# Kernel optimization log

Measured on AMD Instinct MI355X. Metric: run time of the kernel, lower is better.

The kernel has to match this reference:

```python
import jax, jax.numpy as jnp
import numpy as np

N_NODES = 100000
N_EDGES = 1600000
F_IN, HIDDEN, N_CLASS = 64, 48, 40


def setup_inputs() -> dict:
    key = jax.random.key(0)
    ks = jax.random.split(key, 9)
    def glorot(k, fi, fo):
        s = (6.0 / (fi + fo)) ** 0.5
        return jax.random.uniform(k, (fi, fo), jnp.float32, -s, s)
    return {
        "x": jax.random.normal(ks[0], (N_NODES, F_IN), jnp.float32),
        "edge_index": jax.random.randint(ks[1], (2, N_EDGES), 0, N_NODES, jnp.int64),
        "edge_weight": jax.random.uniform(ks[2], (N_EDGES,), jnp.float32),
        "W1": glorot(ks[3], F_IN, HIDDEN),   # ARMAConv init_weight (K=1)
        "V1": glorot(ks[4], F_IN, HIDDEN),   # ARMAConv root_weight
        "b1": jnp.zeros((HIDDEN,), jnp.float32),
        "W2": glorot(ks[5], HIDDEN, N_CLASS),
        "V2": glorot(ks[6], HIDDEN, N_CLASS),
        "b2": jnp.zeros((N_CLASS,), jnp.float32),
    }


def _arma_conv(x, W, V, b, src, dst, norm, num_nodes):
    # out = ReLU( A_norm @ (x @ W) + x @ V + b )   (num_stacks=1, num_layers=1)
    h = x @ W                                   # [N, F_out]
    msg = h[src] * norm[:, None]                # gather + scale  [E, F_out]
    agg = jax.ops.segment_sum(msg, dst, num_segments=num_nodes)  # scatter-add
    return jax.nn.relu(agg + x @ V + b)


def reference(x, edge_index, edge_weight, W1, V1, b1, W2, V2, b2):
    num_nodes = x.shape[0]
    src, dst = edge_index[0], edge_index[1]
    # gcn_norm, add_self_loops=False: D^{-1/2} A D^{-1/2}
    deg = jax.ops.segment_sum(edge_weight, dst, num_segments=num_nodes)
    dinv = jnp.where(deg > 0, jax.lax.rsqrt(jnp.where(deg > 0, deg, 1.0)), 0.0)
    norm = dinv[src] * edge_weight * dinv[dst]
    # eval mode: input dropout is identity
    h = _arma_conv(x, W1, V1, b1, src, dst, norm, num_nodes)
    h = _arma_conv(h, W2, V2, b2, src, dst, norm, num_nodes)
    return jax.nn.log_softmax(h, axis=-1)
```

## Files before the change

### kernel.cpp

```cpp
#include <hip/hip_runtime.h>
#include <math.h>


constexpr int F_IN = 64;
constexpr int HIDDEN = 48;
constexpr int N_CLASS = 40;
constexpr int CHUNK = 8192;
constexpr int BIN_SHIFT = 9;
constexpr int BIN_CAP = 9216;
constexpr int CSR_CAP = 12288;

typedef __attribute__((ext_vector_type(8))) short bf16x8;
typedef __attribute__((ext_vector_type(4))) float f32x4;

__device__ __forceinline__ short bfr(float f) {
    unsigned u = __float_as_uint(f);
    return (short)((u + 0x7fffu + ((u >> 16) & 1u)) >> 16);
}
__device__ __forceinline__ unsigned pack_bf2(float a, float b) {
    unsigned ua = __float_as_uint(a), ub = __float_as_uint(b);
    ua = (ua + 0x7fffu + ((ua >> 16) & 1u)) >> 16;
    ub = (ub + 0x7fffu + ((ub >> 16) & 1u)) >> 16;
    return ua | (ub << 16);
}
__device__ __forceinline__ float2 unpack_bf2(unsigned u) {
    return make_float2(__uint_as_float(u << 16), __uint_as_float(u & 0xffff0000u));
}
__device__ __forceinline__ bf16x8 cvt8(float4 f0, float4 f1) {
    bf16x8 r;
    r[0] = bfr(f0.x); r[1] = bfr(f0.y); r[2] = bfr(f0.z); r[3] = bfr(f0.w);
    r[4] = bfr(f1.x); r[5] = bfr(f1.y); r[6] = bfr(f1.z); r[7] = bfr(f1.w);
    return r;
}

__global__ void init_cursor(int* __restrict__ binCursor) {
    binCursor[threadIdx.x] = (int)threadIdx.x * BIN_CAP;
}

__global__ __launch_bounds__(256) void gemm1_kernel(
    const float* __restrict__ X, const float* __restrict__ W,
    const float* __restrict__ V, const float* __restrict__ b,
    unsigned* __restrict__ XWp, unsigned* __restrict__ AGGp, int N) {
    __shared__ char smem[36864];
    short* sWT = (short*)smem;
    float* ep = (float*)(smem + 12288);
    int tid = threadIdx.x;
    for (int i = tid; i < 96 * 64; i += 256) {
        int c = i >> 6, k = i & 63;
        float v = (c < 48) ? W[k * 48 + c] : V[k * 48 + (c - 48)];
        sWT[i] = bfr(v);
    }
    __syncthreads();

    int lane = tid & 63, wv = tid >> 6;
    int m = lane & 15, quad = lane >> 4;
    int nb0 = (int)blockIdx.x * 64;
    int n = nb0 + wv * 16 + m;

    bf16x8 a0, a1;
    if (n < N) {
        const float4* xr = (const float4*)(X + (size_t)n * 64 + quad * 8);
        a0 = cvt8(xr[0], xr[1]);
        const float4* xr2 = (const float4*)(X + (size_t)n * 64 + 32 + quad * 8);
        a1 = cvt8(xr2[0], xr2[1]);
    } else {
        for (int j = 0; j < 8; ++j) { a0[j] = 0; a1[j] = 0; }
    }

    f32x4 acc[6];
#pragma unroll
    for (int ct = 0; ct < 6; ++ct) acc[ct] = (f32x4){0.f, 0.f, 0.f, 0.f};
#pragma unroll
    for (int ct = 0; ct < 6; ++ct) {
        bf16x8 b0 = *(const bf16x8*)(sWT + (ct * 16 + m) * 64 + quad * 8);
        bf16x8 b1 = *(const bf16x8*)(sWT + (ct * 16 + m) * 64 + 32 + quad * 8);
        acc[ct] = __builtin_amdgcn_mfma_f32_16x16x32_bf16(a0, b0, acc[ct], 0, 0, 0);
        acc[ct] = __builtin_amdgcn_mfma_f32_16x16x32_bf16(a1, b1, acc[ct], 0, 0, 0);
    }
#pragma unroll
    for (int ct = 0; ct < 6; ++ct)
#pragma unroll
        for (int r = 0; r < 4; ++r)
            ep[(wv * 16 + quad * 4 + r) * 96 + ct * 16 + m] = acc[ct][r];
    __syncthreads();
    for (int i = tid; i < 64 * 24; i += 256) {
        int r = i / 24, c2 = i - r * 24;
        int node = nb0 + r;
        if (node >= N) continue;
        float w0 = ep[r * 96 + 2 * c2], w1 = ep[r * 96 + 2 * c2 + 1];
        XWp[node * 24 + c2] = pack_bf2(w0, w1);
        float v0 = ep[r * 96 + 48 + 2 * c2], v1 = ep[r * 96 + 48 + 2 * c2 + 1];
        float2 bb = ((const float2*)b)[c2];
        AGGp[node * 24 + c2] = pack_bf2(v0 + bb.x, v1 + bb.y);
    }
}

__global__ __launch_bounds__(256) void binscatter(
    const int* __restrict__ src, const int* __restrict__ dst,
    const float* __restrict__ w, int* __restrict__ binCursor,
    int2* __restrict__ binned, int E) {
    __shared__ int sx[CHUNK];
    __shared__ int sw[CHUNK];
    __shared__ unsigned char sbin[CHUNK];
    __shared__ int hist[256];
    int tid = threadIdx.x;
    hist[tid] = 0;
    __syncthreads();
    long long e0 = (long long)blockIdx.x * CHUNK;
    int M = (int)min((long long)CHUNK, (long long)E - e0);
    for (int i = tid; i < M; i += 256) {
        int d = dst[e0 + i];
        int bn = d >> BIN_SHIFT;
        sx[i] = ((d & 511) << 17) | src[e0 + i];
        sw[i] = __float_as_int(w[e0 + i]);
        sbin[i] = (unsigned char)bn;
        atomicAdd(&hist[bn], 1);
    }
    __syncthreads();
    int base = atomicAdd(&binCursor[tid], hist[tid]);
    __syncthreads();
    hist[tid] = base;
    __syncthreads();
    for (int i = tid; i < M; i += 256) {
        int p = atomicAdd(&hist[sbin[i]], 1);
        binned[p] = make_int2(sx[i], sw[i]);
    }
}

__global__ __launch_bounds__(512) void build_csr(const int2* __restrict__ binned,
                                                 const int* __restrict__ binCursor,
                                                 int* __restrict__ rowBeg,
                                                 int* __restrict__ rowEnd,
                                                 float* __restrict__ dinv,
                                                 unsigned* __restrict__ csr,
                                                 unsigned* __restrict__ XW1p, int N) {
    __shared__ int sx[CSR_CAP];
    __shared__ int sw[CSR_CAP];
    __shared__ int cntL[512];
    __shared__ float degL[512];
    __shared__ int scanL[512];
    int b = blockIdx.x, tid = threadIdx.x;
    int e0 = b * BIN_CAP;
    int M = min(binCursor[b] - e0, BIN_CAP);
    cntL[tid] = 0;
    degL[tid] = 0.f;
    __syncthreads();
    for (int i = tid; i < M; i += 512) {
        int2 p = binned[e0 + i];
        sx[i] = p.x;
        sw[i] = p.y;
        int dl = ((unsigned)p.x) >> 17;
        atomicAdd(&cntL[dl], 1);
        atomicAdd(&degL[dl], __int_as_float(p.y));
    }
    __syncthreads();
    int v = cntL[tid];
    scanL[tid] = v;
    __syncthreads();
#pragma unroll
    for (int o = 1; o < 512; o <<= 1) {
        int u = (tid >= o) ? scanL[tid - o] : 0;
        __syncthreads();
        scanL[tid] += u;
        __syncthreads();
    }
    int excl = scanL[tid] - v;
    int node = (b << BIN_SHIFT) + tid;
    float dg = degL[tid];
    float dv = dg > 0.f ? rsqrtf(dg) : 0.f;
    if (node < N) {
        rowBeg[node] = e0 + excl;
        rowEnd[node] = e0 + excl + v;
        dinv[node] = dv;
    }
    cntL[tid] = e0 + excl;
    degL[tid] = dv;
    __syncthreads();
    for (int i = tid; i < M; i += 512) {
        int px = sx[i], pw = sw[i];
        int dl = ((unsigned)px) >> 17;
        int pos = atomicAdd(&cntL[dl], 1);
        float wn = __int_as_float(pw) * degL[dl];
        unsigned uw = __float_as_uint(wn);
        uw = (uw + 0x7fffu + ((uw >> 16) & 1u)) >> 16;
        csr[pos] = ((unsigned)(px & 0x1FFFF) << 15) | uw;
    }
    int nb0 = b << BIN_SHIFT;
    for (int i = tid; i < 512 * 24; i += 512) {
        int nl = i / 24, c = i - nl * 24;
        int nn = nb0 + nl;
        if (nn >= N) break;
        float dvn = degL[nl];
        float2 u = unpack_bf2(XW1p[nn * 24 + c]);
        XW1p[nn * 24 + c] = pack_bf2(u.x * dvn, u.y * dvn);
    }
}

template <int W>
__device__ __forceinline__ float4 row_accum2(const unsigned* __restrict__ XWp,
                                             const unsigned* __restrict__ csr,
                                             int j, int end, int c, float4 s) {
    while (j < end && (j & 3)) {
        unsigned p = csr[j++];
        uint2 u = *(const uint2*)(XWp + (p >> 15) * W + c);
        float nr = __uint_as_float((p & 0x7FFFu) << 16);
        float2 x0 = unpack_bf2(u.x), x1 = unpack_bf2(u.y);
        s.x = fmaf(x0.x, nr, s.x); s.y = fmaf(x0.y, nr, s.y);
        s.z = fmaf(x1.x, nr, s.z); s.w = fmaf(x1.y, nr, s.w);
    }
    for (; j + 4 <= end; j += 4) {
        uint4 p4 = *(const uint4*)(csr + j);
        uint2 u0 = *(const uint2*)(XWp + (p4.x >> 15) * W + c);
        uint2 u1 = *(const uint2*)(XWp + (p4.y >> 15) * W + c);
        uint2 u2 = *(const uint2*)(XWp + (p4.z >> 15) * W + c);
        uint2 u3 = *(const uint2*)(XWp + (p4.w >> 15) * W + c);
        float n0 = __uint_as_float((p4.x & 0x7FFFu) << 16);
        float n1 = __uint_as_float((p4.y & 0x7FFFu) << 16);
        float n2 = __uint_as_float((p4.z & 0x7FFFu) << 16);
        float n3 = __uint_as_float((p4.w & 0x7FFFu) << 16);
        float2 a0 = unpack_bf2(u0.x), b0 = unpack_bf2(u0.y);
        float2 a1 = unpack_bf2(u1.x), b1 = unpack_bf2(u1.y);
        float2 a2 = unpack_bf2(u2.x), b2 = unpack_bf2(u2.y);
        float2 a3 = unpack_bf2(u3.x), b3 = unpack_bf2(u3.y);
        s.x = fmaf(a0.x, n0, s.x); s.y = fmaf(a0.y, n0, s.y);
        s.z = fmaf(b0.x, n0, s.z); s.w = fmaf(b0.y, n0, s.w);
        s.x = fmaf(a1.x, n1, s.x); s.y = fmaf(a1.y, n1, s.y);
        s.z = fmaf(b1.x, n1, s.z); s.w = fmaf(b1.y, n1, s.w);
        s.x = fmaf(a2.x, n2, s.x); s.y = fmaf(a2.y, n2, s.y);
        s.z = fmaf(b2.x, n2, s.z); s.w = fmaf(b2.y, n2, s.w);
        s.x = fmaf(a3.x, n3, s.x); s.y = fmaf(a3.y, n3, s.y);
        s.z = fmaf(b3.x, n3, s.z); s.w = fmaf(b3.y, n3, s.w);
    }
    for (; j < end; ++j) {
        unsigned p = csr[j];
        uint2 u = *(const uint2*)(XWp + (p >> 15) * W + c);
        float nr = __uint_as_float((p & 0x7FFFu) << 16);
        float2 x0 = unpack_bf2(u.x), x1 = unpack_bf2(u.y);
        s.x = fmaf(x0.x, nr, s.x); s.y = fmaf(x0.y, nr, s.y);
        s.z = fmaf(x1.x, nr, s.z); s.w = fmaf(x1.y, nr, s.w);
    }
    return s;
}

__global__ __launch_bounds__(384) void pull_agg(const unsigned* __restrict__ XWp,
                                                const unsigned* __restrict__ csr,
                                                const int* __restrict__ rowBeg,
                                                const int* __restrict__ rowEnd,
                                                const unsigned* __restrict__ AGG1p,
                                                unsigned* __restrict__ H1p, int N) {
    int t = blockIdx.x * blockDim.x + threadIdx.x;
    int n = t / 12, c1 = t - n * 12;
    if (n >= N) return;
    int c = 2 * c1;
    uint2 a = *(const uint2*)(AGG1p + n * 24 + c);
    float2 f0 = unpack_bf2(a.x), f1 = unpack_bf2(a.y);
    float4 s = make_float4(f0.x, f0.y, f1.x, f1.y);
    s = row_accum2<24>(XWp, csr, rowBeg[n], rowEnd[n], c, s);
    uint2 o;
    o.x = pack_bf2(fmaxf(s.x, 0.f), fmaxf(s.y, 0.f));
    o.y = pack_bf2(fmaxf(s.z, 0.f), fmaxf(s.w, 0.f));
    *(uint2*)(H1p + n * 24 + c) = o;
}

__global__ __launch_bounds__(256) void gemm2_kernel(
    const short* __restrict__ H1, const float* __restrict__ W,
    const float* __restrict__ V, const float* __restrict__ b,
    const float* __restrict__ dinv, unsigned* __restrict__ XWp,
    unsigned* __restrict__ AGGp, int N) {
    __shared__ char smem[30720];
    short* sWT = (short*)smem;
    float* ep = (float*)(smem + 10240);
    int tid = threadIdx.x;
    for (int i = tid; i < 80 * 64; i += 256) {
        int c = i >> 6, k = i & 63;
        float v = 0.f;
        if (k < 48) v = (c < 40) ? W[k * 40 + c] : V[k * 40 + (c - 40)];
        sWT[i] = bfr(v);
    }
    __syncthreads();

    int lane = tid & 63, wv = tid >> 6;
    int m = lane & 15, quad = lane >> 4;
    int nb0 = (int)blockIdx.x * 64;
    int n = nb0 + wv * 16 + m;

    bf16x8 a0, a1;
    if (n < N) {
        a0 = *(const bf16x8*)(H1 + (size_t)n * 48 + quad * 8);
        if (quad < 2) {
            a1 = *(const bf16x8*)(H1 + (size_t)n * 48 + 32 + quad * 8);
        } else {
            for (int j = 0; j < 8; ++j) a1[j] = 0;
        }
    } else {
        for (int j = 0; j < 8; ++j) { a0[j] = 0; a1[j] = 0; }
    }

    f32x4 acc[5];
#pragma unroll
    for (int ct = 0; ct < 5; ++ct) acc[ct] = (f32x4){0.f, 0.f, 0.f, 0.f};
#pragma unroll
    for (int ct = 0; ct < 5; ++ct) {
        bf16x8 b0 = *(const bf16x8*)(sWT + (ct * 16 + m) * 64 + quad * 8);
        bf16x8 b1 = *(const bf16x8*)(sWT + (ct * 16 + m) * 64 + 32 + quad * 8);
        acc[ct] = __builtin_amdgcn_mfma_f32_16x16x32_bf16(a0, b0, acc[ct], 0, 0, 0);
        acc[ct] = __builtin_amdgcn_mfma_f32_16x16x32_bf16(a1, b1, acc[ct], 0, 0, 0);
    }
#pragma unroll
    for (int ct = 0; ct < 5; ++ct)
#pragma unroll
        for (int r = 0; r < 4; ++r)
            ep[(wv * 16 + quad * 4 + r) * 80 + ct * 16 + m] = acc[ct][r];
    __syncthreads();
    for (int i = tid; i < 64 * 20; i += 256) {
        int r = i / 20, c2 = i - r * 20;
        int node = nb0 + r;
        if (node >= N) continue;
        float dv = dinv[node];
        float w0 = ep[r * 80 + 2 * c2], w1 = ep[r * 80 + 2 * c2 + 1];
        XWp[node * 20 + c2] = pack_bf2(w0 * dv, w1 * dv);
        float v0 = ep[r * 80 + 40 + 2 * c2], v1 = ep[r * 80 + 40 + 2 * c2 + 1];
        float2 bb = ((const float2*)b)[c2];
        AGGp[node * 20 + c2] = pack_bf2(v0 + bb.x, v1 + bb.y);
    }
}

__global__ __launch_bounds__(320) void pull_ls(const unsigned* __restrict__ XWp,
                                               const unsigned* __restrict__ csr,
                                               const int* __restrict__ rowBeg,
                                               const int* __restrict__ rowEnd,
                                               const unsigned* __restrict__ AGG2p,
                                               float* __restrict__ out, int N) {
    __shared__ float4 sbuf[32 * 10];
    __shared__ float sl[32];
    int tid = threadIdx.x;
    int nl = tid / 10, c1 = tid - nl * 10;
    int n = blockIdx.x * 32 + nl;
    int c = 2 * c1;
    float4 s = make_float4(0.f, 0.f, 0.f, 0.f);
    if (n < N) {
        uint2 a = *(const uint2*)(AGG2p + n * 20 + c);
        float2 f0 = unpack_bf2(a.x), f1 = unpack_bf2(a.y);
        s = make_float4(f0.x, f0.y, f1.x, f1.y);
        s = row_accum2<20>(XWp, csr, rowBeg[n], rowEnd[n], c, s);
    }
    sbuf[nl * 10 + c1] = s;
    __syncthreads();
    if (tid < 32) {
        float m = 0.f;
        for (int k = 0; k < 10; ++k) {
            float4 v = sbuf[tid * 10 + k];
            m = fmaxf(m, fmaxf(fmaxf(v.x, v.y), fmaxf(v.z, v.w)));
        }
        float sum = 0.f;
        for (int k = 0; k < 10; ++k) {
            float4 v = sbuf[tid * 10 + k];
            sum += expf(fmaxf(v.x, 0.f) - m) + expf(fmaxf(v.y, 0.f) - m) +
                   expf(fmaxf(v.z, 0.f) - m) + expf(fmaxf(v.w, 0.f) - m);
        }
        sl[tid] = m + logf(sum);
    }
    __syncthreads();
    if (n < N) {
        float l = sl[nl];
        ((float4*)out)[n * 10 + c1] =
            make_float4(fmaxf(s.x, 0.f) - l, fmaxf(s.y, 0.f) - l,
                        fmaxf(s.z, 0.f) - l, fmaxf(s.w, 0.f) - l);
    }
}

extern "C" void kernel_launch(void* const* d_in, const int* in_sizes, int n_in,
                              void* d_out, int out_size, void* d_ws, size_t ws_size,
                              hipStream_t stream) {
    const float* x  = (const float*)d_in[0];
    const int*   ei = (const int*)d_in[1];
    const float* ew = (const float*)d_in[2];
    const float* W1 = (const float*)d_in[3];
    const float* V1 = (const float*)d_in[4];
    const float* b1 = (const float*)d_in[5];
    const float* W2 = (const float*)d_in[6];
    const float* V2 = (const float*)d_in[7];
    const float* b2 = (const float*)d_in[8];
    float* out = (float*)d_out;

    const int N = in_sizes[0] / F_IN;
    const int E = in_sizes[2];
    const int* src = ei;
    const int* dst = ei + E;

    char* ws = (char*)d_ws;
    size_t off = 0;
    auto carve = [&](size_t bytes) {
        void* p = ws + off;
        off = (off + bytes + 255) & ~size_t(255);
        return p;
    };
    int*      binCursor = (int*)carve(256 * 4);
    int*      rowBeg    = (int*)carve((size_t)N * 4);
    int*      rowEnd    = (int*)carve((size_t)N * 4);
    float*    dinv      = (float*)carve((size_t)N * 4);
    int2*     binned    = (int2*)carve((size_t)256 * BIN_CAP * 8);
    unsigned* csr       = (unsigned*)carve((size_t)256 * BIN_CAP * 4);
    unsigned* xW1p      = (unsigned*)carve((size_t)N * 24 * 4);
    unsigned* agg1p     = (unsigned*)carve((size_t)N * 24 * 4);
    unsigned* h1p       = (unsigned*)carve((size_t)N * 24 * 4);
    unsigned* xW2p      = (unsigned*)carve((size_t)N * 20 * 4);
    unsigned* agg2p     = (unsigned*)carve((size_t)N * 20 * 4);

    const int B = 256;
    auto cdiv = [](long long a, long long b) { return (int)((a + b - 1) / b); };
    const int nSc = cdiv(E, CHUNK);
    const int nBins = (N + (1 << BIN_SHIFT) - 1) >> BIN_SHIFT;
    const int nGemmBlocks = cdiv(N, 64);

    init_cursor<<<1, 256, 0, stream>>>(binCursor);
    binscatter<<<nSc, B, 0, stream>>>(src, dst, ew, binCursor, binned, E);
    gemm1_kernel<<<nGemmBlocks, B, 0, stream>>>(x, W1, V1, b1, xW1p, agg1p, N);
    build_csr<<<nBins, 512, 0, stream>>>(binned, binCursor, rowBeg, rowEnd,
                                         dinv, csr, xW1p, N);

    pull_agg<<<cdiv((long long)N * 12, 384), 384, 0, stream>>>(xW1p, csr, rowBeg,
                                                               rowEnd, agg1p, h1p, N);

    gemm2_kernel<<<nGemmBlocks, B, 0, stream>>>((const short*)h1p, W2, V2, b2,
                                                dinv, xW2p, agg2p, N);

    pull_ls<<<cdiv(N, 32), 320, 0, stream>>>(xW2p, csr, rowBeg, rowEnd,
                                             agg2p, out, N);
}
```

Baseline: 275.2 us.

## Split each node's edge list across two lanes in pull aggregation kernels

Both pull kernels (layer 1 aggregation and layer 2 with log-softmax) now assign two threads per feature-pair slice of a node. The two threads interleave 4-edge chunks of the CSR row and combine their partial sums with a lane shuffle. This doubles the thread count and the number of independent gather streams, aiming to hide gather latency on rows of about 16 edges. In exchange it adds shuffle and branching work, duplicate CSR index loads per lane pair, and narrower per-thread writes.

New measurement: 293.4 us. +6.6%, slower.

```diff
diff --git a/kernel.cpp b/kernel.cpp
--- a/kernel.cpp
+++ b/kernel.cpp
@@ -197,18 +197,24 @@
 }
 
 template <int W>
-__device__ __forceinline__ float4 row_accum2(const unsigned* __restrict__ XWp,
-                                             const unsigned* __restrict__ csr,
-                                             int j, int end, int c, float4 s) {
-    while (j < end && (j & 3)) {
-        unsigned p = csr[j++];
-        uint2 u = *(const uint2*)(XWp + (p >> 15) * W + c);
-        float nr = __uint_as_float((p & 0x7FFFu) << 16);
-        float2 x0 = unpack_bf2(u.x), x1 = unpack_bf2(u.y);
-        s.x = fmaf(x0.x, nr, s.x); s.y = fmaf(x0.y, nr, s.y);
-        s.z = fmaf(x1.x, nr, s.z); s.w = fmaf(x1.y, nr, s.w);
-    }
-    for (; j + 4 <= end; j += 4) {
+__device__ __forceinline__ float4 row_accum_split(const unsigned* __restrict__ XWp,
+                                                  const unsigned* __restrict__ csr,
+                                                  int beg, int end, int s, int c,
+                                                  float4 acc) {
+    int ja = min((beg + 3) & ~3, end);
+    if (s == 0) {
+        for (int j = beg; j < ja; ++j) {
+            unsigned p = csr[j];
+            uint2 u = *(const uint2*)(XWp + (p >> 15) * W + c);
+            float nr = __uint_as_float((p & 0x7FFFu) << 16);
+            float2 x0 = unpack_bf2(u.x), x1 = unpack_bf2(u.y);
+            acc.x = fmaf(x0.x, nr, acc.x); acc.y = fmaf(x0.y, nr, acc.y);
+            acc.z = fmaf(x1.x, nr, acc.z); acc.w = fmaf(x1.y, nr, acc.w);
+        }
+    }
+    int nch = (end - ja) >> 2;
+    for (int ck = s; ck < nch; ck += 2) {
+        int j = ja + 4 * ck;
         uint4 p4 = *(const uint4*)(csr + j);
         uint2 u0 = *(const uint2*)(XWp + (p4.x >> 15) * W + c);
         uint2 u1 = *(const uint2*)(XWp + (p4.y >> 15) * W + c);
@@ -222,24 +228,27 @@
         float2 a1 = unpack_bf2(u1.x), b1 = unpack_bf2(u1.y);
         float2 a2 = unpack_bf2(u2.x), b2 = unpack_bf2(u2.y);
         float2 a3 = unpack_bf2(u3.x), b3 = unpack_bf2(u3.y);
-        s.x = fmaf(a0.x, n0, s.x); s.y = fmaf(a0.y, n0, s.y);
-        s.z = fmaf(b0.x, n0, s.z); s.w = fmaf(b0.y, n0, s.w);
-        s.x = fmaf(a1.x, n1, s.x); s.y = fmaf(a1.y, n1, s.y);
-        s.z = fmaf(b1.x, n1, s.z); s.w = fmaf(b1.y, n1, s.w);
-        s.x = fmaf(a2.x, n2, s.x); s.y = fmaf(a2.y, n2, s.y);
-        s.z = fmaf(b2.x, n2, s.z); s.w = fmaf(b2.y, n2, s.w);
-        s.x = fmaf(a3.x, n3, s.x); s.y = fmaf(a3.y, n3, s.y);
-        s.z = fmaf(b3.x, n3, s.z); s.w = fmaf(b3.y, n3, s.w);
-    }
-    for (; j < end; ++j) {
-        unsigned p = csr[j];
-        uint2 u = *(const uint2*)(XWp + (p >> 15) * W + c);
-        float nr = __uint_as_float((p & 0x7FFFu) << 16);
-        float2 x0 = unpack_bf2(u.x), x1 = unpack_bf2(u.y);
-        s.x = fmaf(x0.x, nr, s.x); s.y = fmaf(x0.y, nr, s.y);
-        s.z = fmaf(x1.x, nr, s.z); s.w = fmaf(x1.y, nr, s.w);
-    }
-    return s;
+        acc.x = fmaf(a0.x, n0, acc.x); acc.y = fmaf(a0.y, n0, acc.y);
+        acc.z = fmaf(b0.x, n0, acc.z); acc.w = fmaf(b0.y, n0, acc.w);
+        acc.x = fmaf(a1.x, n1, acc.x); acc.y = fmaf(a1.y, n1, acc.y);
+        acc.z = fmaf(b1.x, n1, acc.z); acc.w = fmaf(b1.y, n1, acc.w);
+        acc.x = fmaf(a2.x, n2, acc.x); acc.y = fmaf(a2.y, n2, acc.y);
+        acc.z = fmaf(b2.x, n2, acc.z); acc.w = fmaf(b2.y, n2, acc.w);
+        acc.x = fmaf(a3.x, n3, acc.x); acc.y = fmaf(a3.y, n3, acc.y);
+        acc.z = fmaf(b3.x, n3, acc.z); acc.w = fmaf(b3.y, n3, acc.w);
+    }
+    int jt = ja + (nch << 2);
+    if ((nch & 1) == s) {
+        for (int j = jt; j < end; ++j) {
+            unsigned p = csr[j];
+            uint2 u = *(const uint2*)(XWp + (p >> 15) * W + c);
+            float nr = __uint_as_float((p & 0x7FFFu) << 16);
+            float2 x0 = unpack_bf2(u.x), x1 = unpack_bf2(u.y);
+            acc.x = fmaf(x0.x, nr, acc.x); acc.y = fmaf(x0.y, nr, acc.y);
+            acc.z = fmaf(x1.x, nr, acc.z); acc.w = fmaf(x1.y, nr, acc.w);
+        }
+    }
+    return acc;
 }
 
 __global__ __launch_bounds__(384) void pull_agg(const unsigned* __restrict__ XWp,
@@ -248,18 +257,25 @@
                                                 const int* __restrict__ rowEnd,
                                                 const unsigned* __restrict__ AGG1p,
                                                 unsigned* __restrict__ H1p, int N) {
-    int t = blockIdx.x * blockDim.x + threadIdx.x;
-    int n = t / 12, c1 = t - n * 12;
-    if (n >= N) return;
-    int c = 2 * c1;
-    uint2 a = *(const uint2*)(AGG1p + n * 24 + c);
-    float2 f0 = unpack_bf2(a.x), f1 = unpack_bf2(a.y);
-    float4 s = make_float4(f0.x, f0.y, f1.x, f1.y);
-    s = row_accum2<24>(XWp, csr, rowBeg[n], rowEnd[n], c, s);
-    uint2 o;
-    o.x = pack_bf2(fmaxf(s.x, 0.f), fmaxf(s.y, 0.f));
-    o.y = pack_bf2(fmaxf(s.z, 0.f), fmaxf(s.w, 0.f));
-    *(uint2*)(H1p + n * 24 + c) = o;
+    int t = blockIdx.x * 384 + threadIdx.x;
+    int n = t / 24, sub = t - n * 24;
+    int c1 = sub >> 1, s = sub & 1, c = 2 * c1;
+    float4 acc = make_float4(0.f, 0.f, 0.f, 0.f);
+    if (n < N) {
+        unsigned a = AGG1p[n * 24 + c + s];
+        float2 f = unpack_bf2(a);
+        if (s == 0) { acc.x = f.x; acc.y = f.y; } else { acc.z = f.x; acc.w = f.y; }
+        acc = row_accum_split<24>(XWp, csr, rowBeg[n], rowEnd[n], s, c, acc);
+    }
+    acc.x += __shfl_xor(acc.x, 1);
+    acc.y += __shfl_xor(acc.y, 1);
+    acc.z += __shfl_xor(acc.z, 1);
+    acc.w += __shfl_xor(acc.w, 1);
+    if (n < N) {
+        unsigned o = (s == 0) ? pack_bf2(fmaxf(acc.x, 0.f), fmaxf(acc.y, 0.f))
+                              : pack_bf2(fmaxf(acc.z, 0.f), fmaxf(acc.w, 0.f));
+        H1p[n * 24 + c + s] = o;
+    }
 }
 
 __global__ __launch_bounds__(256) void gemm2_kernel(
@@ -331,22 +347,26 @@
                                                const int* __restrict__ rowEnd,
                                                const unsigned* __restrict__ AGG2p,
                                                float* __restrict__ out, int N) {
-    __shared__ float4 sbuf[32 * 10];
-    __shared__ float sl[32];
+    __shared__ float4 sbuf[16 * 10];
+    __shared__ float sl[16];
     int tid = threadIdx.x;
-    int nl = tid / 10, c1 = tid - nl * 10;
-    int n = blockIdx.x * 32 + nl;
-    int c = 2 * c1;
-    float4 s = make_float4(0.f, 0.f, 0.f, 0.f);
-    if (n < N) {
-        uint2 a = *(const uint2*)(AGG2p + n * 20 + c);
-        float2 f0 = unpack_bf2(a.x), f1 = unpack_bf2(a.y);
-        s = make_float4(f0.x, f0.y, f1.x, f1.y);
-        s = row_accum2<20>(XWp, csr, rowBeg[n], rowEnd[n], c, s);
-    }
-    sbuf[nl * 10 + c1] = s;
-    __syncthreads();
-    if (tid < 32) {
+    int nl = tid / 20, sub = tid - nl * 20;
+    int c1 = sub >> 1, s = sub & 1, c = 2 * c1;
+    int n = blockIdx.x * 16 + nl;
+    float4 acc = make_float4(0.f, 0.f, 0.f, 0.f);
+    if (n < N) {
+        unsigned a = AGG2p[n * 20 + c + s];
+        float2 f = unpack_bf2(a);
+        if (s == 0) { acc.x = f.x; acc.y = f.y; } else { acc.z = f.x; acc.w = f.y; }
+        acc = row_accum_split<20>(XWp, csr, rowBeg[n], rowEnd[n], s, c, acc);
+    }
+    acc.x += __shfl_xor(acc.x, 1);
+    acc.y += __shfl_xor(acc.y, 1);
+    acc.z += __shfl_xor(acc.z, 1);
+    acc.w += __shfl_xor(acc.w, 1);
+    if (s == 0) sbuf[nl * 10 + c1] = acc;
+    __syncthreads();
+    if (tid < 16) {
         float m = 0.f;
         for (int k = 0; k < 10; ++k) {
             float4 v = sbuf[tid * 10 + k];
@@ -363,9 +383,9 @@
     __syncthreads();
     if (n < N) {
         float l = sl[nl];
-        ((float4*)out)[n * 10 + c1] =
-            make_float4(fmaxf(s.x, 0.f) - l, fmaxf(s.y, 0.f) - l,
-                        fmaxf(s.z, 0.f) - l, fmaxf(s.w, 0.f) - l);
+        float2 o = (s == 0) ? make_float2(fmaxf(acc.x, 0.f) - l, fmaxf(acc.y, 0.f) - l)
+                            : make_float2(fmaxf(acc.z, 0.f) - l, fmaxf(acc.w, 0.f) - l);
+        *(float2*)(out + (size_t)n * 40 + 4 * c1 + 2 * s) = o;
     }
 }
 
@@ -419,12 +439,12 @@
     build_csr<<<nBins, 512, 0, stream>>>(binned, binCursor, rowBeg, rowEnd,
                                          dinv, csr, xW1p, N);
 
-    pull_agg<<<cdiv((long long)N * 12, 384), 384, 0, stream>>>(xW1p, csr, rowBeg,
+    pull_agg<<<cdiv((long long)N * 24, 384), 384, 0, stream>>>(xW1p, csr, rowBeg,
                                                                rowEnd, agg1p, h1p, N);
 
     gemm2_kernel<<<nGemmBlocks, B, 0, stream>>>((const short*)h1p, W2, V2, b2,
                                                 dinv, xW2p, agg2p, N);
 
-    pull_ls<<<cdiv(N, 32), 320, 0, stream>>>(xW2p, csr, rowBeg, rowEnd,
+    pull_ls<<<cdiv(N, 16), 320, 0, stream>>>(xW2p, csr, rowBeg, rowEnd,
                                              agg2p, out, N);
 }
```
